# Kernel optimization log

Measured on AMD Instinct MI355X. Metric: run time of the kernel, lower is better.

The kernel has to match this reference:

```python
import jax, jax.numpy as jnp
import numpy as np

N_VALUES = 4
N_DIGITS = 7
N_CLASSES = 10
INPUT_DIM = 2048
BATCH = 32768


def setup_inputs() -> dict:
    key = jax.random.key(0)
    k1, k2, k3, k4 = jax.random.split(key, 4)
    hidden = jax.random.normal(k1, (BATCH, INPUT_DIM), dtype=jnp.float32)
    labels = jax.random.randint(k2, (BATCH, N_VALUES, N_DIGITS), 0, N_CLASSES, dtype=jnp.int64)
    H = N_VALUES * N_DIGITS  # 28 heads
    # nn.Linear default init: U(-1/sqrt(fan_in), 1/sqrt(fan_in))
    bound = 1.0 / np.sqrt(INPUT_DIM)
    W = jax.random.uniform(k3, (H, N_CLASSES, INPUT_DIM), minval=-bound, maxval=bound, dtype=jnp.float32)
    b = jax.random.uniform(k4, (H, N_CLASSES), minval=-bound, maxval=bound, dtype=jnp.float32)
    return {"hidden": hidden, "labels": labels, "W": W, "b": b}


def reference(hidden, labels, W, b):
    B = hidden.shape[0]
    # Fuse all 28 tiny GEMMs into one: [B,D] x [H,C,D] -> [B,H,C]
    logits = jnp.einsum('bd,hcd->bhc', hidden, W) + b  # [B, 28, 10]
    logits = logits.reshape(B, N_VALUES, N_DIGITS, N_CLASSES)
    # per-head cross entropy (mean over batch), summed over heads, / (n_values*n_digits)
    logp = jax.nn.log_softmax(logits, axis=-1)  # [B, V, D, C]
    nll = -jnp.take_along_axis(logp, labels[..., None], axis=-1)[..., 0]  # [B, V, D]
    loss = jnp.mean(nll, axis=0).sum() / (N_VALUES * N_DIGITS)
    return loss, logits
```

## Files before the change

kernel.cpp:

```cpp
#include <hip/hip_runtime.h>
#include <hip/hip_bf16.h>

#define BATCH   32768
#define DIM     2048
#define NHEADS  28
#define NCOLS   280
#define LOSS_SCALE (1.0f / (float)(BATCH * NHEADS))

typedef __attribute__((ext_vector_type(8))) short short8;
typedef __attribute__((ext_vector_type(4))) short s4vec;
typedef __attribute__((ext_vector_type(4))) float f32x4;

__device__ __forceinline__ short f2bf(float f) {
    union { __hip_bfloat16 h; short s; } u; u.h = __float2bfloat16(f); return u.s;
}

__global__ void mvh_swz(const float* __restrict__ W, short* __restrict__ Wswz) {
    int t = blockIdx.x * 256 + threadIdx.x;
    int lane = t & 63;
    int ks = (t >> 6) & 63;
    int nt = t >> 12;
    int n = nt * 16 + (lane & 15);
    int d = ks * 32 + (lane >> 4) * 8;
    short8 v;
    #pragma unroll
    for (int j = 0; j < 8; j++) v[j] = 0;
    if (n < NCOLS) {
        const float* src = W + (size_t)n * DIM + d;
        #pragma unroll
        for (int j = 0; j < 8; j++) v[j] = f2bf(src[j]);
    }
    *(short8*)(Wswz + (size_t)t * 8) = v;
}

#define B_TILE 18432
#define AB(b)  ((b) * 8192)
#define BB(b)  (16384 + (b) * B_TILE)
#define CL_PITCH 292

#define SB0() __builtin_amdgcn_sched_barrier(0)
#define WAITV(N) asm volatile("s_waitcnt vmcnt(" #N ") lgkmcnt(0)" ::: "memory")
#define BARN(N) do { SB0(); WAITV(N); __builtin_amdgcn_s_barrier(); SB0(); } while (0)

__global__ __launch_bounds__(512, 4)
void mvh_gemm(const float* __restrict__ hidden, const short* __restrict__ Wswz,
              const float* __restrict__ bias, float* __restrict__ logits,
              const int* __restrict__ labels, float* __restrict__ loss_out) {
    __shared__ __align__(16) char lds[53248];

    const int tid  = threadIdx.x;
    const int lane = tid & 63;
    const int wave = tid >> 6;
    const int kph   = wave >> 2;
    const int wsub  = (wave >> 1) & 1;
    const int nhalf = wave & 1;
    const int l15 = lane & 15, lhi = lane >> 4;
    const int rowbase = blockIdx.x * 64;

    const int ar  = tid >> 3;
    const int ak4 = (tid & 7) * 4;
    const float* gAbase = hidden + (size_t)(rowbase + ar) * DIM + ak4;
    const int awbyte = (ar >> 4) * 1024 + ((ar & 15) + 16 * (ak4 >> 3)) * 16 + (ak4 & 4) * 2;

    f32x4 acc0[9], acc1[9];
    #pragma unroll
    for (int n = 0; n < 9; n++) { acc0[n] = (f32x4)0.0f; acc1[n] = (f32x4)0.0f; }

    f32x4 ga0, ga1;

#define LOADA2(grp) do { \
    const float* p_ = gAbase + (size_t)(grp) * 64; \
    ga0 = *(const f32x4*)(p_); \
    ga1 = *(const f32x4*)(p_ + 32); \
    SB0(); \
} while (0)

#define WRA1(dstoff, slot, src) do { \
    s4vec w_; \
    w_[0] = f2bf(src[0]); w_[1] = f2bf(src[1]); w_[2] = f2bf(src[2]); w_[3] = f2bf(src[3]); \
    *(s4vec*)(lds + (dstoff) + (slot) * 4096 + awbyte) = w_; \
} while (0)

#define WRITEA2(dstoff) do { WRA1(dstoff, 0, ga0); WRA1(dstoff, 1, ga1); } while (0)

#define STAGE_B(dstoff, kt) do { \
    _Pragma("unroll") \
    for (int i_ = 0; i_ < 3; i_++) { \
        if (i_ < 2 || tid < 128) { \
            int g_ = (i_ < 2) ? (i_ * 512 + tid) : (1024 + tid); \
            const short* gp_ = Wswz + (size_t)((g_ >> 6) * 64 + (kt)) * 512 + (g_ & 63) * 8; \
            __builtin_amdgcn_global_load_lds((const __attribute__((address_space(1))) void*)gp_, \
                (__attribute__((address_space(3))) void*)(lds + (dstoff) + g_ * 16), 16, 0, 0); \
        } \
    } \
    SB0(); \
} while (0)

#define COMPUTE(aoff, boff) do { \
    short8 af0_ = *(const short8*)(lds + (aoff) + (wsub * 2 + 0) * 1024 + lane * 16); \
    short8 af1_ = *(const short8*)(lds + (aoff) + (wsub * 2 + 1) * 1024 + lane * 16); \
    _Pragma("unroll") \
    for (int n_ = 0; n_ < 9; n_++) { \
        short8 bf_ = *(const short8*)(lds + (boff) + (nhalf * 9 + n_) * 1024 + lane * 16); \
        acc0[n_] = __builtin_amdgcn_mfma_f32_16x16x32_bf16(af0_, bf_, acc0[n_], 0, 0, 0); \
        acc1[n_] = __builtin_amdgcn_mfma_f32_16x16x32_bf16(af1_, bf_, acc1[n_], 0, 0, 0); \
    } \
} while (0)

    LOADA2(0);
    WRITEA2(AB(0));
    STAGE_B(BB(0), 0);
    BARN(0);

    #pragma unroll 1
    for (int g = 0; g < 32; g++) {
        const int t0 = g * 2;
        const int ac = AB(g & 1);
        const int an = AB((g & 1) ^ 1);
        STAGE_B(BB(1), t0 + 1);
        if (g < 31) LOADA2(g + 1);
        if (kph == 0) COMPUTE(ac, BB(0));
        if (g < 31) { BARN(2); } else { BARN(0); }
        if (g < 31) STAGE_B(BB(0), t0 + 2);
        if (kph == 1) COMPUTE(ac + 4096, BB(1));
        SB0();
        if (g < 31) WRITEA2(an);
        BARN(0);
    }

#undef LOADA2
#undef WRA1
#undef WRITEA2
#undef STAGE_B
#undef COMPUTE

    float* Cl  = (float*)lds;
    float* red = (float*)(lds + 38912);
    float lsum = 0.0f;

    #pragma unroll 1
    for (int s = 0; s < 2; s++) {
        __syncthreads();
        if (kph == 1 && wsub == s) {
            #pragma unroll
            for (int nf = 0; nf < 9; nf++) {
                int c = nhalf * 144 + nf * 16 + l15;
                #pragma unroll
                for (int r = 0; r < 4; r++) {
                    Cl[(lhi * 4 + r) * CL_PITCH + c]      = acc0[nf][r];
                    Cl[(16 + lhi * 4 + r) * CL_PITCH + c] = acc1[nf][r];
                }
            }
        }
        __syncthreads();
        if (kph == 0 && wsub == s) {
            #pragma unroll
            for (int nf = 0; nf < 9; nf++) {
                int c = nhalf * 144 + nf * 16 + l15;
                #pragma unroll
                for (int r = 0; r < 4; r++) {
                    Cl[(lhi * 4 + r) * CL_PITCH + c]      += acc0[nf][r];
                    Cl[(16 + lhi * 4 + r) * CL_PITCH + c] += acc1[nf][r];
                }
            }
        }
        __syncthreads();
        #pragma unroll 1
        for (int i = tid; i < 32 * 70; i += 512) {
            int lr = i / 70, ch = i - lr * 70;
            f32x4 v  = *(const f32x4*)(Cl + lr * CL_PITCH + ch * 4);
            f32x4 bv = *(const f32x4*)(bias + ch * 4);
            *(f32x4*)(logits + (size_t)(rowbase + s * 32 + lr) * NCOLS + ch * 4) = v + bv;
        }
        #pragma unroll 1
        for (int p = tid; p < 32 * NHEADS; p += 512) {
            int lr = p / NHEADS, h = p - lr * NHEADS;
            const float* x  = Cl + lr * CL_PITCH + h * 10;
            const float* bb = bias + h * 10;
            float xv[10];
            #pragma unroll
            for (int j = 0; j < 10; j++) xv[j] = x[j] + bb[j];
            float mx = xv[0];
            #pragma unroll
            for (int j = 1; j < 10; j++) mx = fmaxf(mx, xv[j]);
            float sm = 0.0f;
            #pragma unroll
            for (int j = 0; j < 10; j++) sm += __expf(xv[j] - mx);
            int lab = labels[(size_t)(rowbase + s * 32 + lr) * NHEADS + h];
            float xl = xv[0];
            #pragma unroll
            for (int j = 1; j < 10; j++) xl = (lab == j) ? xv[j] : xl;
            lsum += mx + __logf(sm) - xl;
        }
    }

    #pragma unroll
    for (int off = 32; off > 0; off >>= 1)
        lsum += __shfl_down(lsum, off, 64);
    if (lane == 0) red[wave] = lsum;
    __syncthreads();
    if (tid == 0) {
        float t = red[0] + red[1] + red[2] + red[3]
                + red[4] + red[5] + red[6] + red[7];
        atomicAdd(loss_out, t * LOSS_SCALE);
    }
}

extern "C" void kernel_launch(void* const* d_in, const int* in_sizes, int n_in,
                              void* d_out, int out_size, void* d_ws, size_t ws_size,
                              hipStream_t stream) {
    const float* hidden = (const float*)d_in[0];
    const int* labels   = (const int*)d_in[1];
    const float* W      = (const float*)d_in[2];
    const float* bias   = (const float*)d_in[3];
    float* out = (float*)d_out;
    short* Wswz = (short*)d_ws;

    (void)hipMemsetAsync(d_out, 0, sizeof(float), stream);
    mvh_swz<<<288, 256, 0, stream>>>(W, Wswz);
    mvh_gemm<<<512, 512, 0, stream>>>(hidden, Wswz, bias, out + 1, labels, out);
}
```

Baseline: 102.6 us.

## Load A fragments directly into registers, bypassing LDS staging

Each wave now loads its own hidden-row fragments from global memory straight into registers and converts them to bf16 right before the MFMAs, so the A tile is no longer staged through LDS. This removes the LDS writes and reads for A, shrinks the shared-memory footprint, and cuts the barriers per iteration from three to two, using per-k-phase waitcnt values. The trade-off is that global loads for A are now uncoalesced across lanes (16 rows × 32-byte pieces) and load latency must be hidden by register prefetch only one step ahead.

```diff
diff --git a/kernel.cpp b/kernel.cpp
--- a/kernel.cpp
+++ b/kernel.cpp
@@ -8,7 +8,6 @@
 #define LOSS_SCALE (1.0f / (float)(BATCH * NHEADS))
 
 typedef __attribute__((ext_vector_type(8))) short short8;
-typedef __attribute__((ext_vector_type(4))) short s4vec;
 typedef __attribute__((ext_vector_type(4))) float f32x4;
 
 __device__ __forceinline__ short f2bf(float f) {
@@ -33,20 +32,24 @@
     *(short8*)(Wswz + (size_t)t * 8) = v;
 }
 
-#define B_TILE 18432
-#define AB(b)  ((b) * 8192)
-#define BB(b)  (16384 + (b) * B_TILE)
+#define BB(b)  ((b) * 18432)
 #define CL_PITCH 292
 
 #define SB0() __builtin_amdgcn_sched_barrier(0)
-#define WAITV(N) asm volatile("s_waitcnt vmcnt(" #N ") lgkmcnt(0)" ::: "memory")
-#define BARN(N) do { SB0(); WAITV(N); __builtin_amdgcn_s_barrier(); SB0(); } while (0)
+#define BARV(kpar) do { \
+    SB0(); \
+    if (kph == (kpar)) { asm volatile("s_waitcnt vmcnt(4) lgkmcnt(0)" ::: "memory"); } \
+    else               { asm volatile("s_waitcnt vmcnt(0) lgkmcnt(0)" ::: "memory"); } \
+    __builtin_amdgcn_s_barrier(); SB0(); \
+} while (0)
+#define BAR0() do { SB0(); asm volatile("s_waitcnt vmcnt(0) lgkmcnt(0)" ::: "memory"); \
+    __builtin_amdgcn_s_barrier(); SB0(); } while (0)
 
 __global__ __launch_bounds__(512, 4)
 void mvh_gemm(const float* __restrict__ hidden, const short* __restrict__ Wswz,
               const float* __restrict__ bias, float* __restrict__ logits,
               const int* __restrict__ labels, float* __restrict__ loss_out) {
-    __shared__ __align__(16) char lds[53248];
+    __shared__ __align__(16) char lds[38944];
 
     const int tid  = threadIdx.x;
     const int lane = tid & 63;
@@ -57,31 +60,22 @@
     const int l15 = lane & 15, lhi = lane >> 4;
     const int rowbase = blockIdx.x * 64;
 
-    const int ar  = tid >> 3;
-    const int ak4 = (tid & 7) * 4;
-    const float* gAbase = hidden + (size_t)(rowbase + ar) * DIM + ak4;
-    const int awbyte = (ar >> 4) * 1024 + ((ar & 15) + 16 * (ak4 >> 3)) * 16 + (ak4 & 4) * 2;
+    const float* paBase = hidden + (size_t)(rowbase + wsub * 32 + l15) * DIM + lhi * 8;
 
     f32x4 acc0[9], acc1[9];
     #pragma unroll
     for (int n = 0; n < 9; n++) { acc0[n] = (f32x4)0.0f; acc1[n] = (f32x4)0.0f; }
 
-    f32x4 ga0, ga1;
-
-#define LOADA2(grp) do { \
-    const float* p_ = gAbase + (size_t)(grp) * 64; \
-    ga0 = *(const f32x4*)(p_); \
-    ga1 = *(const f32x4*)(p_ + 32); \
+    f32x4 pa0, pa1, pa2, pa3;
+
+#define LOADPA(t) do { \
+    const float* p_ = paBase + (t) * 32; \
+    pa0 = *(const f32x4*)(p_); \
+    pa1 = *(const f32x4*)(p_ + 4); \
+    pa2 = *(const f32x4*)(p_ + (size_t)16 * DIM); \
+    pa3 = *(const f32x4*)(p_ + (size_t)16 * DIM + 4); \
     SB0(); \
 } while (0)
-
-#define WRA1(dstoff, slot, src) do { \
-    s4vec w_; \
-    w_[0] = f2bf(src[0]); w_[1] = f2bf(src[1]); w_[2] = f2bf(src[2]); w_[3] = f2bf(src[3]); \
-    *(s4vec*)(lds + (dstoff) + (slot) * 4096 + awbyte) = w_; \
-} while (0)
-
-#define WRITEA2(dstoff) do { WRA1(dstoff, 0, ga0); WRA1(dstoff, 1, ga1); } while (0)
 
 #define STAGE_B(dstoff, kt) do { \
     _Pragma("unroll") \
@@ -96,9 +90,13 @@
     SB0(); \
 } while (0)
 
-#define COMPUTE(aoff, boff) do { \
-    short8 af0_ = *(const short8*)(lds + (aoff) + (wsub * 2 + 0) * 1024 + lane * 16); \
-    short8 af1_ = *(const short8*)(lds + (aoff) + (wsub * 2 + 1) * 1024 + lane * 16); \
+#define COMPUTE(boff) do { \
+    short8 af0_, af1_; \
+    _Pragma("unroll") \
+    for (int j_ = 0; j_ < 4; j_++) { \
+        af0_[j_] = f2bf(pa0[j_]); af0_[4 + j_] = f2bf(pa1[j_]); \
+        af1_[j_] = f2bf(pa2[j_]); af1_[4 + j_] = f2bf(pa3[j_]); \
+    } \
     _Pragma("unroll") \
     for (int n_ = 0; n_ < 9; n_++) { \
         short8 bf_ = *(const short8*)(lds + (boff) + (nhalf * 9 + n_) * 1024 + lane * 16); \
@@ -107,30 +105,27 @@
     } \
 } while (0)
 
-    LOADA2(0);
-    WRITEA2(AB(0));
     STAGE_B(BB(0), 0);
-    BARN(0);
+    if (kph == 0) LOADPA(0); else LOADPA(1);
+    SB0();
+    asm volatile("s_waitcnt vmcnt(4) lgkmcnt(0)" ::: "memory");
+    __builtin_amdgcn_s_barrier();
+    SB0();
 
     #pragma unroll 1
     for (int g = 0; g < 32; g++) {
         const int t0 = g * 2;
-        const int ac = AB(g & 1);
-        const int an = AB((g & 1) ^ 1);
+        if (kph == 0) COMPUTE(BB(0));
         STAGE_B(BB(1), t0 + 1);
-        if (g < 31) LOADA2(g + 1);
-        if (kph == 0) COMPUTE(ac, BB(0));
-        if (g < 31) { BARN(2); } else { BARN(0); }
+        if (kph == 0 && g < 31) LOADPA(t0 + 2);
+        if (g < 31) { BARV(0); } else { BAR0(); }
+        if (kph == 1) COMPUTE(BB(1));
         if (g < 31) STAGE_B(BB(0), t0 + 2);
-        if (kph == 1) COMPUTE(ac + 4096, BB(1));
-        SB0();
-        if (g < 31) WRITEA2(an);
-        BARN(0);
-    }
-
-#undef LOADA2
-#undef WRA1
-#undef WRITEA2
+        if (kph == 1 && g < 31) LOADPA(t0 + 3);
+        if (g < 31) { BARV(1); } else { BAR0(); }
+    }
+
+#undef LOADPA
 #undef STAGE_B
 #undef COMPUTE
 
```

Result: slower. 130.7 us (+27.3%).

## Triple-buffer B tiles and interleave A loads per k-step with per-wave vmcnt waits

Applied to the files above, without the earlier changes.

Restructures the main loop so each half-iteration prefetches one A chunk and one B k-tile two steps ahead, using a three-slot rotating B buffer in LDS instead of double buffering. Barriers now wait with partial vmcnt counts that differ by wave, since only some waves issue the third B load. The goal is deeper overlap of global loads with MFMA compute and fewer stalls at barriers. The cost is more LDS per block, which may lower occupancy, and more barriers per iteration.

```diff
diff --git a/kernel.cpp b/kernel.cpp
--- a/kernel.cpp
+++ b/kernel.cpp
@@ -33,20 +33,23 @@
     *(short8*)(Wswz + (size_t)t * 8) = v;
 }
 
-#define B_TILE 18432
-#define AB(b)  ((b) * 8192)
-#define BB(b)  (16384 + (b) * B_TILE)
+#define BO(k)  (8192 + ((k) % 3) * 18432)
 #define CL_PITCH 292
 
 #define SB0() __builtin_amdgcn_sched_barrier(0)
-#define WAITV(N) asm volatile("s_waitcnt vmcnt(" #N ") lgkmcnt(0)" ::: "memory")
-#define BARN(N) do { SB0(); WAITV(N); __builtin_amdgcn_s_barrier(); SB0(); } while (0)
+#define BARV() do { SB0(); \
+    if (wave < 2) { asm volatile("s_waitcnt vmcnt(4) lgkmcnt(0)" ::: "memory"); } \
+    else          { asm volatile("s_waitcnt vmcnt(3) lgkmcnt(0)" ::: "memory"); } \
+    __builtin_amdgcn_s_barrier(); SB0(); \
+} while (0)
+#define BAR0() do { SB0(); asm volatile("s_waitcnt vmcnt(0) lgkmcnt(0)" ::: "memory"); \
+    __builtin_amdgcn_s_barrier(); SB0(); } while (0)
 
 __global__ __launch_bounds__(512, 4)
 void mvh_gemm(const float* __restrict__ hidden, const short* __restrict__ Wswz,
               const float* __restrict__ bias, float* __restrict__ logits,
               const int* __restrict__ labels, float* __restrict__ loss_out) {
-    __shared__ __align__(16) char lds[53248];
+    __shared__ __align__(16) char lds[63488];
 
     const int tid  = threadIdx.x;
     const int lane = tid & 63;
@@ -59,38 +62,31 @@
 
     const int ar  = tid >> 3;
     const int ak4 = (tid & 7) * 4;
-    const float* gAbase = hidden + (size_t)(rowbase + ar) * DIM + ak4;
+    const float* gA1 = hidden + (size_t)(rowbase + ar) * DIM + ak4;
     const int awbyte = (ar >> 4) * 1024 + ((ar & 15) + 16 * (ak4 >> 3)) * 16 + (ak4 & 4) * 2;
 
     f32x4 acc0[9], acc1[9];
     #pragma unroll
     for (int n = 0; n < 9; n++) { acc0[n] = (f32x4)0.0f; acc1[n] = (f32x4)0.0f; }
 
-    f32x4 ga0, ga1;
-
-#define LOADA2(grp) do { \
-    const float* p_ = gAbase + (size_t)(grp) * 64; \
-    ga0 = *(const f32x4*)(p_); \
-    ga1 = *(const f32x4*)(p_ + 32); \
-    SB0(); \
-} while (0)
-
-#define WRA1(dstoff, slot, src) do { \
+    f32x4 gx, gy;
+
+#define LOADA1(reg, t) do { reg = *(const f32x4*)(gA1 + (t) * 32); SB0(); } while (0)
+
+#define WRITEA1(aoff, reg) do { \
     s4vec w_; \
-    w_[0] = f2bf(src[0]); w_[1] = f2bf(src[1]); w_[2] = f2bf(src[2]); w_[3] = f2bf(src[3]); \
-    *(s4vec*)(lds + (dstoff) + (slot) * 4096 + awbyte) = w_; \
-} while (0)
-
-#define WRITEA2(dstoff) do { WRA1(dstoff, 0, ga0); WRA1(dstoff, 1, ga1); } while (0)
-
-#define STAGE_B(dstoff, kt) do { \
+    w_[0] = f2bf(reg[0]); w_[1] = f2bf(reg[1]); w_[2] = f2bf(reg[2]); w_[3] = f2bf(reg[3]); \
+    *(s4vec*)(lds + (aoff) + awbyte) = w_; \
+} while (0)
+
+#define STAGE_B(boff, kt) do { \
     _Pragma("unroll") \
     for (int i_ = 0; i_ < 3; i_++) { \
         if (i_ < 2 || tid < 128) { \
             int g_ = (i_ < 2) ? (i_ * 512 + tid) : (1024 + tid); \
             const short* gp_ = Wswz + (size_t)((g_ >> 6) * 64 + (kt)) * 512 + (g_ & 63) * 8; \
             __builtin_amdgcn_global_load_lds((const __attribute__((address_space(1))) void*)gp_, \
-                (__attribute__((address_space(3))) void*)(lds + (dstoff) + g_ * 16), 16, 0, 0); \
+                (__attribute__((address_space(3))) void*)(lds + (boff) + g_ * 16), 16, 0, 0); \
         } \
     } \
     SB0(); \
@@ -107,30 +103,30 @@
     } \
 } while (0)
 
-    LOADA2(0);
-    WRITEA2(AB(0));
-    STAGE_B(BB(0), 0);
-    BARN(0);
+    LOADA1(gx, 0);
+    STAGE_B(BO(0), 0);
+    WRITEA1(0, gx);
+    LOADA1(gy, 1);
+    STAGE_B(BO(1), 1);
+    BARV();
 
     #pragma unroll 1
-    for (int g = 0; g < 32; g++) {
-        const int t0 = g * 2;
-        const int ac = AB(g & 1);
-        const int an = AB((g & 1) ^ 1);
-        STAGE_B(BB(1), t0 + 1);
-        if (g < 31) LOADA2(g + 1);
-        if (kph == 0) COMPUTE(ac, BB(0));
-        if (g < 31) { BARN(2); } else { BARN(0); }
-        if (g < 31) STAGE_B(BB(0), t0 + 2);
-        if (kph == 1) COMPUTE(ac + 4096, BB(1));
+    for (int tp = 0; tp < 32; tp++) {
+        const int t = tp * 2;
+        if (tp < 31) { LOADA1(gx, t + 2); STAGE_B(BO(t + 2), t + 2); }
+        if (kph == 0) COMPUTE(0, BO(t));
         SB0();
-        if (g < 31) WRITEA2(an);
-        BARN(0);
-    }
-
-#undef LOADA2
-#undef WRA1
-#undef WRITEA2
+        WRITEA1(4096, gy);
+        if (tp < 31) { BARV(); } else { BAR0(); }
+        if (tp < 31) { LOADA1(gy, t + 3); STAGE_B(BO(t + 3), t + 3); }
+        if (kph == 1) COMPUTE(4096, BO(t + 1));
+        SB0();
+        if (tp < 31) WRITEA1(0, gx);
+        if (tp < 31) { BARV(); } else { BAR0(); }
+    }
+
+#undef LOADA1
+#undef WRITEA1
 #undef STAGE_B
 #undef COMPUTE
 
```

Result: no change. 104.3 us (+1.6%).
